# Performance work log

Measured on AMD Instinct MI355X. Metric: run time of the kernel, lower is better.

## Reference

```python
import jax, jax.numpy as jnp
import numpy as np

C = 64

def conv1x1(W, b, x):
    # W: [out, in], b: [out], x: [B, in, N, K] -> [B, out, N, K]
    return jnp.einsum('oc,bcnk->bonk', W, x) + b[None, :, None, None]

def setup_inputs() -> dict:
    key = jax.random.key(0)
    ks = jax.random.split(key, 20)
    B, N, K = 8, 4096, 16
    def w(k, o, i):
        # kaiming-uniform-ish init like torch Conv2d default
        bound = 1.0 / np.sqrt(i)
        return jax.random.uniform(k, (o, i), jnp.float32, -bound, bound)
    def bias(k, o, i):
        bound = 1.0 / np.sqrt(i)
        return jax.random.uniform(k, (o,), jnp.float32, -bound, bound)
    inp = {
        'grouped_xyz': jax.random.normal(ks[0], (B, 3, N, K), jnp.float32),
        'grouped_feature': jax.random.normal(ks[1], (B, C, N, K), jnp.float32),
        'kW': w(ks[2], C, C), 'kb': bias(ks[3], C, C),
        'vW': w(ks[4], C, C), 'vb': bias(ks[5], C, C),
        'pm1W': w(ks[6], C, 3), 'pm1b': bias(ks[7], C, 3),
        'pm2W': w(ks[8], C, C), 'pm2b': bias(ks[9], C, C),
        'pb1W': w(ks[10], C, 3), 'pb1b': bias(ks[11], C, 3),
        'pb2W': w(ks[12], C, C), 'pb2b': bias(ks[13], C, C),
        'we1W': w(ks[14], C, C), 'we1b': bias(ks[15], C, C),
        'we2W': w(ks[16], C, C), 'we2b': bias(ks[17], C, C),
        'resW': w(ks[18], C, C), 'resb': bias(ks[19], C, C),
    }
    return inp

def reference(grouped_xyz, grouped_feature, kW, kb, vW, vb,
              pm1W, pm1b, pm2W, pm2b, pb1W, pb1b, pb2W, pb2b,
              we1W, we1b, we2W, we2b, resW, resb):
    key = conv1x1(kW, kb, grouped_feature)
    value = conv1x1(vW, vb, grouped_feature)
    # positional-encoding multiplier and bias (Conv-ReLU-Conv on xyz)
    pem = conv1x1(pm2W, pm2b, jax.nn.relu(conv1x1(pm1W, pm1b, grouped_xyz)))
    peb = conv1x1(pb2W, pb2b, jax.nn.relu(conv1x1(pb1W, pb1b, grouped_xyz)))
    relation_qk = key * pem + peb
    value = value + peb
    weight = conv1x1(we2W, we2b, jax.nn.relu(conv1x1(we1W, we1b, relation_qk)))
    score = jax.nn.softmax(weight, axis=2)  # softmax over npoint dim, as in source
    feature = score * value
    # residual_emb: ReLU then 1x1 conv
    return conv1x1(resW, resb, jax.nn.relu(feature))
```

## Files before the change

### kernel.cpp

```cpp
#include <hip/hip_runtime.h>
#include <hip/hip_fp16.h>

#define NKr 65536
#define LOG2E 1.44269504f

typedef __attribute__((ext_vector_type(4))) float f32x4;
typedef __attribute__((ext_vector_type(8))) short s16x8;

__device__ __forceinline__ short bfc(float x){
    union{float f; unsigned u;} a; a.f = x;
    unsigned r = a.u + 0x7fffu + ((a.u >> 16) & 1u);
    return (short)(r >> 16);
}
__device__ __forceinline__ short hfc(float x){
    __half h = __float2half(x);
    return *(short*)&h;
}
__device__ __forceinline__ float hdec(unsigned short s){
    __half h = *(__half*)&s;
    return __half2float(h);
}

__global__ void k0_kernel(const float* __restrict__ pm1W, const float* __restrict__ pb1W,
                          const float* __restrict__ pm2W, const float* __restrict__ pb2W,
                          const float* __restrict__ kW,   const float* __restrict__ vW,
                          const float* __restrict__ we1W, const float* __restrict__ we2W,
                          const float* __restrict__ resW, short* __restrict__ wbf)
{
    const int tg = blockIdx.x * 256 + threadIdx.x;
    for (int i = tg; i < 32768; i += 16384){
        short v;
        if (i < 2048){
            const int o = i >> 5, c = i & 31;
            v = (c < 3) ? bfc(pm1W[o*3 + c]) : (short)0;
        } else if (i < 4096){
            const int ii = i - 2048, o = ii >> 5, c = ii & 31;
            v = (c < 3) ? bfc(pb1W[o*3 + c]) : (short)0;
        } else {
            const int m = (i - 4096) >> 12, j = (i - 4096) & 4095;
            const float* s = (m == 0) ? pm2W : (m == 1) ? pb2W : (m == 2) ? kW
                           : (m == 3) ? vW   : (m == 4) ? we1W : (m == 5) ? we2W : resW;
            v = bfc(s[j]);
        }
        wbf[i] = v;
    }
}

__device__ __forceinline__ void gemm64(const short* __restrict__ S,
                                       const short* __restrict__ wbf, int wo,
                                       const float* __restrict__ bias,
                                       int li, int hi, f32x4 acc[4][4])
{
#pragma unroll
    for (int mi = 0; mi < 4; ++mi){
        const float4 bv = *(const float4*)(bias + 16*mi + 4*hi);
#pragma unroll
        for (int ni = 0; ni < 4; ++ni){
            acc[mi][ni][0] = bv.x; acc[mi][ni][1] = bv.y;
            acc[mi][ni][2] = bv.z; acc[mi][ni][3] = bv.w;
        }
    }
#pragma unroll
    for (int ks = 0; ks < 2; ++ks){
        s16x8 af[4];
#pragma unroll
        for (int mi = 0; mi < 4; ++mi)
            af[mi] = *(const s16x8*)(wbf + wo + (16*mi + li)*64 + ks*32 + hi*8);
#pragma unroll
        for (int ni = 0; ni < 4; ++ni){
            const int p = 16*ni + li;
            const s16x8 bf_ = *(const s16x8*)(S + ((p*64 + ks*32 + hi*8) ^ ((li & 7) << 3)));
#pragma unroll
            for (int mi = 0; mi < 4; ++mi)
                acc[mi][ni] = __builtin_amdgcn_mfma_f32_16x16x32_bf16(af[mi], bf_, acc[mi][ni], 0, 0, 0);
        }
    }
}

__device__ __forceinline__ void gemm32x(const s16x8* __restrict__ xf,
                                        const short* __restrict__ wbf, int wo,
                                        const float* __restrict__ bias,
                                        int li, int hi, f32x4 acc[4][4])
{
#pragma unroll
    for (int mi = 0; mi < 4; ++mi){
        const float4 bv = *(const float4*)(bias + 16*mi + 4*hi);
#pragma unroll
        for (int ni = 0; ni < 4; ++ni){
            acc[mi][ni][0] = bv.x; acc[mi][ni][1] = bv.y;
            acc[mi][ni][2] = bv.z; acc[mi][ni][3] = bv.w;
        }
    }
    s16x8 af[4];
#pragma unroll
    for (int mi = 0; mi < 4; ++mi)
        af[mi] = *(const s16x8*)(wbf + wo + (16*mi + li)*32 + hi*8);
#pragma unroll
    for (int ni = 0; ni < 4; ++ni)
#pragma unroll
        for (int mi = 0; mi < 4; ++mi)
            acc[mi][ni] = __builtin_amdgcn_mfma_f32_16x16x32_bf16(af[mi], xf[ni], acc[mi][ni], 0, 0, 0);
}

__device__ __forceinline__ void dstore_bf(short* __restrict__ Tt, f32x4 acc[4][4],
                                          int li, int hi, bool relu)
{
#pragma unroll
    for (int mi = 0; mi < 4; ++mi){
        const int o0 = 16*mi + 4*hi;
#pragma unroll
        for (int ni = 0; ni < 4; ++ni){
            const int p = 16*ni + li;
            float a0 = acc[mi][ni][0], a1 = acc[mi][ni][1];
            float a2 = acc[mi][ni][2], a3 = acc[mi][ni][3];
            if (relu){ a0 = fmaxf(a0, 0.f); a1 = fmaxf(a1, 0.f);
                       a2 = fmaxf(a2, 0.f); a3 = fmaxf(a3, 0.f); }
            uint2 pk;
            pk.x = (unsigned)(unsigned short)bfc(a0) | ((unsigned)(unsigned short)bfc(a1) << 16);
            pk.y = (unsigned)(unsigned short)bfc(a2) | ((unsigned)(unsigned short)bfc(a3) << 16);
            *(uint2*)(Tt + ((p*64 + o0) ^ ((li & 7) << 3))) = pk;
        }
    }
}

__device__ __forceinline__ void dstore_h16(short* __restrict__ Tt, f32x4 acc[4][4],
                                           int li, int hi)
{
#pragma unroll
    for (int mi = 0; mi < 4; ++mi){
        const int o0 = 16*mi + 4*hi;
#pragma unroll
        for (int ni = 0; ni < 4; ++ni){
            const int p = 16*ni + li;
            uint2 pk;
            pk.x = (unsigned)(unsigned short)hfc(acc[mi][ni][0]) | ((unsigned)(unsigned short)hfc(acc[mi][ni][1]) << 16);
            pk.y = (unsigned)(unsigned short)hfc(acc[mi][ni][2]) | ((unsigned)(unsigned short)hfc(acc[mi][ni][3]) << 16);
            *(uint2*)(Tt + ((p*64 + o0) ^ ((li & 7) << 3))) = pk;
        }
    }
}

__device__ __forceinline__ void tstore(const short* __restrict__ Tt, short* __restrict__ gout, int l)
{
#pragma unroll
    for (int g = 0; g < 8; ++g){
        uint4 d = *(const uint4*)(Tt + ((l*64 + g*8) ^ ((l & 7) << 3)));
        *(uint4*)(gout + g*8) = d;
    }
}

__global__ void __launch_bounds__(64, 4) k1_kernel(
    const float* __restrict__ xyz, const float* __restrict__ feat,
    const short* __restrict__ wbf,
    const float* __restrict__ kb,  const float* __restrict__ vb,
    const float* __restrict__ pm1b, const float* __restrict__ pm2b,
    const float* __restrict__ pb1b, const float* __restrict__ pb2b,
    const float* __restrict__ we1b, const float* __restrict__ we2b,
    short* __restrict__ o_val2, short* __restrict__ o_wgt)
{
    __shared__ short Fs[4096];
    __shared__ short Ts[4096];
    const int l = threadIdx.x;
    const int li = l & 15, hi = l >> 4;
    short* F = Fs;
    short* T = Ts;
    const int b = blockIdx.x >> 10;
    const int rbase = (blockIdx.x & 1023) << 6;

    {
        const float* fb = feat + (size_t)(b * 64) * NKr + rbase + l;
#pragma unroll 4
        for (int c0 = 0; c0 < 64; c0 += 8){
            short v[8];
#pragma unroll
            for (int j = 0; j < 8; ++j) v[j] = bfc(fb[(size_t)(c0 + j) * NKr]);
            uint4 pk;
            pk.x = (unsigned)(unsigned short)v[0] | ((unsigned)(unsigned short)v[1] << 16);
            pk.y = (unsigned)(unsigned short)v[2] | ((unsigned)(unsigned short)v[3] << 16);
            pk.z = (unsigned)(unsigned short)v[4] | ((unsigned)(unsigned short)v[5] << 16);
            pk.w = (unsigned)(unsigned short)v[6] | ((unsigned)(unsigned short)v[7] << 16);
            *(uint4*)(F + ((l*64 + c0) ^ ((l & 7) << 3))) = pk;
        }
    }
    s16x8 xf[4];
#pragma unroll
    for (int ni = 0; ni < 4; ++ni)
#pragma unroll
        for (int j = 0; j < 8; ++j) xf[ni][j] = 0;
    if (hi == 0){
        const float* xb = xyz + (size_t)(b * 3) * NKr + rbase;
#pragma unroll
        for (int ni = 0; ni < 4; ++ni){
            const int p = 16*ni + li;
            xf[ni][0] = bfc(xb[p]);
            xf[ni][1] = bfc(xb[NKr + p]);
            xf[ni][2] = bfc(xb[2*NKr + p]);
        }
    }

    f32x4 A1[4][4], A2[4][4];
    gemm64(F, wbf, 12288, kb, li, hi, A1);
    gemm32x(xf, wbf, 0, pm1b, li, hi, A2);
    dstore_bf(T, A2, li, hi, true);
    gemm64(T, wbf, 4096, pm2b, li, hi, A2);
#pragma unroll
    for (int mi = 0; mi < 4; ++mi)
#pragma unroll
        for (int ni = 0; ni < 4; ++ni)
#pragma unroll
            for (int j = 0; j < 4; ++j) A1[mi][ni][j] *= A2[mi][ni][j];
    gemm32x(xf, wbf, 2048, pb1b, li, hi, A2);
    dstore_bf(T, A2, li, hi, true);
    gemm64(T, wbf, 8192, pb2b, li, hi, A2);
#pragma unroll
    for (int mi = 0; mi < 4; ++mi)
#pragma unroll
        for (int ni = 0; ni < 4; ++ni)
#pragma unroll
            for (int j = 0; j < 4; ++j) A1[mi][ni][j] += A2[mi][ni][j];
    dstore_bf(T, A1, li, hi, false);
    gemm64(F, wbf, 16384, vb, li, hi, A1);
#pragma unroll
    for (int mi = 0; mi < 4; ++mi)
#pragma unroll
        for (int ni = 0; ni < 4; ++ni)
#pragma unroll
            for (int j = 0; j < 4; ++j) A1[mi][ni][j] += A2[mi][ni][j];
    dstore_h16(F, A1, li, hi);
    const size_t rowoff = ((size_t)b * NKr + rbase + l) * 64;
    tstore(F, o_val2 + rowoff, l);
    gemm64(T, wbf, 20480, we1b, li, hi, A1);
    dstore_bf(F, A1, li, hi, true);
    gemm64(F, wbf, 24576, we2b, li, hi, A1);
    dstore_h16(T, A1, li, hi);
    tstore(T, o_wgt + rowoff, l);
}

__device__ __forceinline__ void comb(float& m, float& S, float mo, float So)
{
    float mn = fmaxf(m, mo);
    S = S * exp2f((m - mn) * LOG2E) + So * exp2f((mo - mn) * LOG2E);
    m = mn;
}

__global__ void __launch_bounds__(512) k2_kernel(const short* __restrict__ wgt,
                                                 float* __restrict__ mstat,
                                                 float* __restrict__ rstat)
{
    __shared__ float redm[8][4][8], reds[8][4][8];
    const int blk = blockIdx.x;
    const int b = blk >> 5, k = (blk >> 1) & 15, h = blk & 1;
    const int t = threadIdx.x;
    const int oct = t & 3, g = t >> 2;
    const short* wp = wgt + (size_t)b * NKr * 64 + (size_t)k * 64 + h * 32 + oct * 8;

    float m[8], S[8];
#pragma unroll
    for (int j = 0; j < 8; ++j){ m[j] = -3.0e38f; S[j] = 0.f; }
#pragma unroll 2
    for (int i = 0; i < 32; ++i){
        const int n = g + 128 * i;
        const uint4 u = *(const uint4*)(wp + (size_t)n * 1024);
        unsigned short hs[8] = {
            (unsigned short)(u.x & 0xffffu), (unsigned short)(u.x >> 16),
            (unsigned short)(u.y & 0xffffu), (unsigned short)(u.y >> 16),
            (unsigned short)(u.z & 0xffffu), (unsigned short)(u.z >> 16),
            (unsigned short)(u.w & 0xffffu), (unsigned short)(u.w >> 16)};
#pragma unroll
        for (int j = 0; j < 8; ++j){
            const float x = hdec(hs[j]);
            const float mn = fmaxf(m[j], x);
            S[j] = S[j] * exp2f((m[j] - mn) * LOG2E) + exp2f((x - mn) * LOG2E);
            m[j] = mn;
        }
    }
#pragma unroll
    for (int d = 4; d <= 32; d <<= 1){
#pragma unroll
        for (int j = 0; j < 8; ++j){
            float mo = __shfl_xor(m[j], d, 64);
            float So = __shfl_xor(S[j], d, 64);
            comb(m[j], S[j], mo, So);
        }
    }
    const int wv = t >> 6, ln = t & 63;
    if (ln < 4){
#pragma unroll
        for (int j = 0; j < 8; ++j){ redm[wv][ln][j] = m[j]; reds[wv][ln][j] = S[j]; }
    }
    __syncthreads();
    if (t < 32){
        const int oc = t >> 3, j = t & 7;
        float M = redm[0][oc][j], Sm = reds[0][oc][j];
#pragma unroll
        for (int wv2 = 1; wv2 < 8; ++wv2) comb(M, Sm, redm[wv2][oc][j], reds[wv2][oc][j]);
        const int idx = (b * 16 + k) * 64 + h * 32 + oc * 8 + j;
        mstat[idx] = M;
        rstat[idx] = 1.0f / Sm;
    }
}

__global__ void __launch_bounds__(64, 4) k3_kernel(
    const short* __restrict__ wgt, const short* __restrict__ val2,
    const float* __restrict__ mstat, const float* __restrict__ rstat,
    const short* __restrict__ wbf, const float* __restrict__ resb,
    float* __restrict__ out)
{
    __shared__ short ftile[4096];
    __shared__ float mls[1024], rls[1024];
    const int l = threadIdx.x;
    const int li = l & 15, hi = l >> 4;
    const int b = blockIdx.x >> 10;
    const int rbase = (blockIdx.x & 1023) << 6;

    {
        const float* mp = mstat + b * 1024;
        const float* rp = rstat + b * 1024;
#pragma unroll
        for (int i = 0; i < 16; ++i){
            const int f = l + 64 * i;
            const int kk = f >> 6;
            const int fs = f ^ ((kk & 7) << 2);
            mls[fs] = mp[f];
            rls[fs] = rp[f];
        }
    }
    __syncthreads();

    short* Ft = ftile;
    const int k = l & 15;
    const size_t rowoff = ((size_t)b * NKr + rbase + l) * 64;
    const short* wp = wgt + rowoff;
    const short* vp = val2 + rowoff;
#pragma unroll 2
    for (int g = 0; g < 8; ++g){
        const uint4 uw = *(const uint4*)(wp + g * 8);
        const uint4 uv = *(const uint4*)(vp + g * 8);
        const int f0 = (k * 64 + g * 8) ^ ((k & 7) << 2);
        const int f1 = (k * 64 + g * 8 + 4) ^ ((k & 7) << 2);
        const float4 m0 = *(const float4*)(mls + f0);
        const float4 m1 = *(const float4*)(mls + f1);
        const float4 r0 = *(const float4*)(rls + f0);
        const float4 r1 = *(const float4*)(rls + f1);
        const unsigned short ws8[8] = {
            (unsigned short)(uw.x & 0xffffu), (unsigned short)(uw.x >> 16),
            (unsigned short)(uw.y & 0xffffu), (unsigned short)(uw.y >> 16),
            (unsigned short)(uw.z & 0xffffu), (unsigned short)(uw.z >> 16),
            (unsigned short)(uw.w & 0xffffu), (unsigned short)(uw.w >> 16)};
        const unsigned short vs8[8] = {
            (unsigned short)(uv.x & 0xffffu), (unsigned short)(uv.x >> 16),
            (unsigned short)(uv.y & 0xffffu), (unsigned short)(uv.y >> 16),
            (unsigned short)(uv.z & 0xffffu), (unsigned short)(uv.z >> 16),
            (unsigned short)(uv.w & 0xffffu), (unsigned short)(uv.w >> 16)};
        const float mv[8] = {m0.x, m0.y, m0.z, m0.w, m1.x, m1.y, m1.z, m1.w};
        const float rv[8] = {r0.x, r0.y, r0.z, r0.w, r1.x, r1.y, r1.z, r1.w};
        short fo[8];
#pragma unroll
        for (int j = 0; j < 8; ++j){
            const float sc = exp2f((hdec(ws8[j]) - mv[j]) * LOG2E) * rv[j];
            fo[j] = bfc(fmaxf(sc * hdec(vs8[j]), 0.f));
        }
        uint4 pk;
        pk.x = (unsigned)(unsigned short)fo[0] | ((unsigned)(unsigned short)fo[1] << 16);
        pk.y = (unsigned)(unsigned short)fo[2] | ((unsigned)(unsigned short)fo[3] << 16);
        pk.z = (unsigned)(unsigned short)fo[4] | ((unsigned)(unsigned short)fo[5] << 16);
        pk.w = (unsigned)(unsigned short)fo[6] | ((unsigned)(unsigned short)fo[7] << 16);
        *(uint4*)(Ft + ((l * 64 + g * 8) ^ ((l & 7) << 3))) = pk;
    }
    f32x4 acc[4][4];
    gemm64(Ft, wbf, 28672, resb, li, hi, acc);
    float* op = out + (size_t)b * 64 * NKr;
#pragma unroll
    for (int mi = 0; mi < 4; ++mi){
        const int o0 = 16 * mi + 4 * hi;
#pragma unroll
        for (int ni = 0; ni < 4; ++ni){
            const int r = rbase + 16 * ni + li;
#pragma unroll
            for (int j = 0; j < 4; ++j)
                op[(size_t)(o0 + j) * NKr + r] = acc[mi][ni][j];
        }
    }
}

extern "C" void kernel_launch(void* const* d_in, const int* in_sizes, int n_in,
                              void* d_out, int out_size, void* d_ws, size_t ws_size,
                              hipStream_t stream)
{
    const float* xyz  = (const float*)d_in[0];
    const float* feat = (const float*)d_in[1];
    const float* kW   = (const float*)d_in[2];  const float* kb   = (const float*)d_in[3];
    const float* vW   = (const float*)d_in[4];  const float* vb   = (const float*)d_in[5];
    const float* pm1W = (const float*)d_in[6];  const float* pm1b = (const float*)d_in[7];
    const float* pm2W = (const float*)d_in[8];  const float* pm2b = (const float*)d_in[9];
    const float* pb1W = (const float*)d_in[10]; const float* pb1b = (const float*)d_in[11];
    const float* pb2W = (const float*)d_in[12]; const float* pb2b = (const float*)d_in[13];
    const float* we1W = (const float*)d_in[14]; const float* we1b = (const float*)d_in[15];
    const float* we2W = (const float*)d_in[16]; const float* we2b = (const float*)d_in[17];
    const float* resW = (const float*)d_in[18]; const float* resb = (const float*)d_in[19];

    short* wbf   = (short*)d_ws;
    float* mstat = (float*)((char*)d_ws + 65536);
    float* rstat = (float*)((char*)d_ws + 98304);
    short* val2  = (short*)((char*)d_ws + 131072);
    short* wgt   = (short*)((char*)d_ws + 131072 + 67108864);

    k0_kernel<<<64, 256, 0, stream>>>(pm1W, pb1W, pm2W, pb2W, kW, vW, we1W, we2W, resW, wbf);
    k1_kernel<<<8192, 64, 0, stream>>>(xyz, feat, wbf, kb, vb, pm1b, pm2b,
                                       pb1b, pb2b, we1b, we2b, val2, wgt);
    k2_kernel<<<256, 512, 0, stream>>>(wgt, mstat, rstat);
    k3_kernel<<<8192, 64, 0, stream>>>(wgt, val2, mstat, rstat, wbf, resb, (float*)d_out);
}
```

Measured before the change: 437.9 us.

## Split 64-row tiles across four waves per block in k1 and k3

The k1 and k3 kernels change from one 64-thread wave per 64-point tile to 256-thread blocks. Each of the four waves computes 16 of the 64 output channels through new per-wave GEMM and store helpers, with __syncthreads between the chained GEMM stages. k3 drops its shared-memory staging of the softmax statistics and reads them directly as float4 per thread, and k1 keeps value results in a third shared buffer. The intent is to cut per-thread accumulator register pressure and get more parallel waves per tile, at the cost of extra barriers and smaller MFMA work per wave.

After: 380.6 us. 1.15x faster.

```diff
diff --git a/kernel.cpp b/kernel.cpp
--- a/kernel.cpp
+++ b/kernel.cpp
@@ -46,110 +46,72 @@
     }
 }
 
-__device__ __forceinline__ void gemm64(const short* __restrict__ S,
-                                       const short* __restrict__ wbf, int wo,
-                                       const float* __restrict__ bias,
-                                       int li, int hi, f32x4 acc[4][4])
-{
-#pragma unroll
-    for (int mi = 0; mi < 4; ++mi){
-        const float4 bv = *(const float4*)(bias + 16*mi + 4*hi);
-#pragma unroll
-        for (int ni = 0; ni < 4; ++ni){
-            acc[mi][ni][0] = bv.x; acc[mi][ni][1] = bv.y;
-            acc[mi][ni][2] = bv.z; acc[mi][ni][3] = bv.w;
-        }
-    }
-#pragma unroll
-    for (int ks = 0; ks < 2; ++ks){
-        s16x8 af[4];
-#pragma unroll
-        for (int mi = 0; mi < 4; ++mi)
-            af[mi] = *(const s16x8*)(wbf + wo + (16*mi + li)*64 + ks*32 + hi*8);
-#pragma unroll
-        for (int ni = 0; ni < 4; ++ni){
-            const int p = 16*ni + li;
-            const s16x8 bf_ = *(const s16x8*)(S + ((p*64 + ks*32 + hi*8) ^ ((li & 7) << 3)));
-#pragma unroll
-            for (int mi = 0; mi < 4; ++mi)
-                acc[mi][ni] = __builtin_amdgcn_mfma_f32_16x16x32_bf16(af[mi], bf_, acc[mi][ni], 0, 0, 0);
-        }
-    }
-}
-
-__device__ __forceinline__ void gemm32x(const s16x8* __restrict__ xf,
+__device__ __forceinline__ void sgemm64(const short* __restrict__ S,
                                         const short* __restrict__ wbf, int wo,
                                         const float* __restrict__ bias,
-                                        int li, int hi, f32x4 acc[4][4])
-{
-#pragma unroll
-    for (int mi = 0; mi < 4; ++mi){
-        const float4 bv = *(const float4*)(bias + 16*mi + 4*hi);
+                                        int w, int li, int hi, f32x4 acc[4])
+{
+    const float4 bv = *(const float4*)(bias + 16*w + 4*hi);
+#pragma unroll
+    for (int ni = 0; ni < 4; ++ni){
+        acc[ni][0] = bv.x; acc[ni][1] = bv.y; acc[ni][2] = bv.z; acc[ni][3] = bv.w;
+    }
+#pragma unroll
+    for (int ks = 0; ks < 2; ++ks){
+        const s16x8 af = *(const s16x8*)(wbf + wo + (16*w + li)*64 + ks*32 + hi*8);
 #pragma unroll
         for (int ni = 0; ni < 4; ++ni){
-            acc[mi][ni][0] = bv.x; acc[mi][ni][1] = bv.y;
-            acc[mi][ni][2] = bv.z; acc[mi][ni][3] = bv.w;
-        }
-    }
-    s16x8 af[4];
-#pragma unroll
-    for (int mi = 0; mi < 4; ++mi)
-        af[mi] = *(const s16x8*)(wbf + wo + (16*mi + li)*32 + hi*8);
+            const s16x8 bf_ = *(const s16x8*)(S + (((16*ni + li)*64 + ks*32 + hi*8) ^ ((li & 7) << 3)));
+            acc[ni] = __builtin_amdgcn_mfma_f32_16x16x32_bf16(af, bf_, acc[ni], 0, 0, 0);
+        }
+    }
+}
+
+__device__ __forceinline__ void sgemm32x(const s16x8* __restrict__ xf,
+                                         const short* __restrict__ wbf, int wo,
+                                         const float* __restrict__ bias,
+                                         int w, int li, int hi, f32x4 acc[4])
+{
+    const float4 bv = *(const float4*)(bias + 16*w + 4*hi);
+#pragma unroll
+    for (int ni = 0; ni < 4; ++ni){
+        acc[ni][0] = bv.x; acc[ni][1] = bv.y; acc[ni][2] = bv.z; acc[ni][3] = bv.w;
+    }
+    const s16x8 af = *(const s16x8*)(wbf + wo + (16*w + li)*32 + hi*8);
 #pragma unroll
     for (int ni = 0; ni < 4; ++ni)
-#pragma unroll
-        for (int mi = 0; mi < 4; ++mi)
-            acc[mi][ni] = __builtin_amdgcn_mfma_f32_16x16x32_bf16(af[mi], xf[ni], acc[mi][ni], 0, 0, 0);
-}
-
-__device__ __forceinline__ void dstore_bf(short* __restrict__ Tt, f32x4 acc[4][4],
-                                          int li, int hi, bool relu)
-{
-#pragma unroll
-    for (int mi = 0; mi < 4; ++mi){
-        const int o0 = 16*mi + 4*hi;
-#pragma unroll
-        for (int ni = 0; ni < 4; ++ni){
-            const int p = 16*ni + li;
-            float a0 = acc[mi][ni][0], a1 = acc[mi][ni][1];
-            float a2 = acc[mi][ni][2], a3 = acc[mi][ni][3];
-            if (relu){ a0 = fmaxf(a0, 0.f); a1 = fmaxf(a1, 0.f);
-                       a2 = fmaxf(a2, 0.f); a3 = fmaxf(a3, 0.f); }
-            uint2 pk;
-            pk.x = (unsigned)(unsigned short)bfc(a0) | ((unsigned)(unsigned short)bfc(a1) << 16);
-            pk.y = (unsigned)(unsigned short)bfc(a2) | ((unsigned)(unsigned short)bfc(a3) << 16);
-            *(uint2*)(Tt + ((p*64 + o0) ^ ((li & 7) << 3))) = pk;
-        }
-    }
-}
-
-__device__ __forceinline__ void dstore_h16(short* __restrict__ Tt, f32x4 acc[4][4],
-                                           int li, int hi)
-{
-#pragma unroll
-    for (int mi = 0; mi < 4; ++mi){
-        const int o0 = 16*mi + 4*hi;
-#pragma unroll
-        for (int ni = 0; ni < 4; ++ni){
-            const int p = 16*ni + li;
-            uint2 pk;
-            pk.x = (unsigned)(unsigned short)hfc(acc[mi][ni][0]) | ((unsigned)(unsigned short)hfc(acc[mi][ni][1]) << 16);
-            pk.y = (unsigned)(unsigned short)hfc(acc[mi][ni][2]) | ((unsigned)(unsigned short)hfc(acc[mi][ni][3]) << 16);
-            *(uint2*)(Tt + ((p*64 + o0) ^ ((li & 7) << 3))) = pk;
-        }
-    }
-}
-
-__device__ __forceinline__ void tstore(const short* __restrict__ Tt, short* __restrict__ gout, int l)
-{
-#pragma unroll
-    for (int g = 0; g < 8; ++g){
-        uint4 d = *(const uint4*)(Tt + ((l*64 + g*8) ^ ((l & 7) << 3)));
-        *(uint4*)(gout + g*8) = d;
-    }
-}
-
-__global__ void __launch_bounds__(64, 4) k1_kernel(
+        acc[ni] = __builtin_amdgcn_mfma_f32_16x16x32_bf16(af, xf[ni], acc[ni], 0, 0, 0);
+}
+
+__device__ __forceinline__ void sdstore_bf(short* __restrict__ T, const f32x4 acc[4],
+                                           int w, int li, int hi, bool relu)
+{
+    const int o0 = 16*w + 4*hi;
+#pragma unroll
+    for (int ni = 0; ni < 4; ++ni){
+        float a0 = acc[ni][0], a1 = acc[ni][1], a2 = acc[ni][2], a3 = acc[ni][3];
+        if (relu){ a0 = fmaxf(a0,0.f); a1 = fmaxf(a1,0.f); a2 = fmaxf(a2,0.f); a3 = fmaxf(a3,0.f); }
+        uint2 pk;
+        pk.x = (unsigned)(unsigned short)bfc(a0) | ((unsigned)(unsigned short)bfc(a1) << 16);
+        pk.y = (unsigned)(unsigned short)bfc(a2) | ((unsigned)(unsigned short)bfc(a3) << 16);
+        *(uint2*)(T + (((16*ni + li)*64 + o0) ^ ((li & 7) << 3))) = pk;
+    }
+}
+
+__device__ __forceinline__ void sdstore_h16(short* __restrict__ T, const f32x4 acc[4],
+                                            int w, int li, int hi)
+{
+    const int o0 = 16*w + 4*hi;
+#pragma unroll
+    for (int ni = 0; ni < 4; ++ni){
+        uint2 pk;
+        pk.x = (unsigned)(unsigned short)hfc(acc[ni][0]) | ((unsigned)(unsigned short)hfc(acc[ni][1]) << 16);
+        pk.y = (unsigned)(unsigned short)hfc(acc[ni][2]) | ((unsigned)(unsigned short)hfc(acc[ni][3]) << 16);
+        *(uint2*)(T + (((16*ni + li)*64 + o0) ^ ((li & 7) << 3))) = pk;
+    }
+}
+
+__global__ void __launch_bounds__(256, 4) k1_kernel(
     const float* __restrict__ xyz, const float* __restrict__ feat,
     const short* __restrict__ wbf,
     const float* __restrict__ kb,  const float* __restrict__ vb,
@@ -158,29 +120,32 @@
     const float* __restrict__ we1b, const float* __restrict__ we2b,
     short* __restrict__ o_val2, short* __restrict__ o_wgt)
 {
-    __shared__ short Fs[4096];
-    __shared__ short Ts[4096];
-    const int l = threadIdx.x;
+    __shared__ short F[4096];
+    __shared__ short T[4096];
+    __shared__ short Vt[4096];
+    const int tid = threadIdx.x;
+    const int w = tid >> 6, l = tid & 63;
     const int li = l & 15, hi = l >> 4;
-    short* F = Fs;
-    short* T = Ts;
     const int b = blockIdx.x >> 10;
     const int rbase = (blockIdx.x & 1023) << 6;
 
     {
-        const float* fb = feat + (size_t)(b * 64) * NKr + rbase + l;
-#pragma unroll 4
-        for (int c0 = 0; c0 < 64; c0 += 8){
-            short v[8];
-#pragma unroll
-            for (int j = 0; j < 8; ++j) v[j] = bfc(fb[(size_t)(c0 + j) * NKr]);
-            uint4 pk;
-            pk.x = (unsigned)(unsigned short)v[0] | ((unsigned)(unsigned short)v[1] << 16);
-            pk.y = (unsigned)(unsigned short)v[2] | ((unsigned)(unsigned short)v[3] << 16);
-            pk.z = (unsigned)(unsigned short)v[4] | ((unsigned)(unsigned short)v[5] << 16);
-            pk.w = (unsigned)(unsigned short)v[6] | ((unsigned)(unsigned short)v[7] << 16);
-            *(uint4*)(F + ((l*64 + c0) ^ ((l & 7) << 3))) = pk;
-        }
+        const float* fb = feat + ((size_t)(b*64 + 16*w)) * NKr + rbase + l;
+        short v[16];
+#pragma unroll
+        for (int j = 0; j < 16; ++j) v[j] = bfc(fb[(size_t)j * NKr]);
+        uint4 p0, p1;
+        p0.x = (unsigned)(unsigned short)v[0] | ((unsigned)(unsigned short)v[1] << 16);
+        p0.y = (unsigned)(unsigned short)v[2] | ((unsigned)(unsigned short)v[3] << 16);
+        p0.z = (unsigned)(unsigned short)v[4] | ((unsigned)(unsigned short)v[5] << 16);
+        p0.w = (unsigned)(unsigned short)v[6] | ((unsigned)(unsigned short)v[7] << 16);
+        p1.x = (unsigned)(unsigned short)v[8] | ((unsigned)(unsigned short)v[9] << 16);
+        p1.y = (unsigned)(unsigned short)v[10] | ((unsigned)(unsigned short)v[11] << 16);
+        p1.z = (unsigned)(unsigned short)v[12] | ((unsigned)(unsigned short)v[13] << 16);
+        p1.w = (unsigned)(unsigned short)v[14] | ((unsigned)(unsigned short)v[15] << 16);
+        const int s0 = l*64 + 16*w;
+        *(uint4*)(F + (s0 ^ ((l & 7) << 3))) = p0;
+        *(uint4*)(F + ((s0 + 8) ^ ((l & 7) << 3))) = p1;
     }
     s16x8 xf[4];
 #pragma unroll
@@ -188,52 +153,71 @@
 #pragma unroll
         for (int j = 0; j < 8; ++j) xf[ni][j] = 0;
     if (hi == 0){
-        const float* xb = xyz + (size_t)(b * 3) * NKr + rbase;
+        const float* xb = xyz + (size_t)(b*3) * NKr + rbase;
 #pragma unroll
         for (int ni = 0; ni < 4; ++ni){
-            const int p = 16*ni + li;
-            xf[ni][0] = bfc(xb[p]);
-            xf[ni][1] = bfc(xb[NKr + p]);
-            xf[ni][2] = bfc(xb[2*NKr + p]);
-        }
-    }
-
-    f32x4 A1[4][4], A2[4][4];
-    gemm64(F, wbf, 12288, kb, li, hi, A1);
-    gemm32x(xf, wbf, 0, pm1b, li, hi, A2);
-    dstore_bf(T, A2, li, hi, true);
-    gemm64(T, wbf, 4096, pm2b, li, hi, A2);
-#pragma unroll
-    for (int mi = 0; mi < 4; ++mi)
+            xf[ni][0] = bfc(xb[16*ni + li]);
+            xf[ni][1] = bfc(xb[NKr + 16*ni + li]);
+            xf[ni][2] = bfc(xb[2*NKr + 16*ni + li]);
+        }
+    }
+    __syncthreads();
+
+    f32x4 V[4], K[4], P[4];
+    sgemm64(F, wbf, 16384, vb, w, li, hi, V);
+    sgemm64(F, wbf, 12288, kb, w, li, hi, K);
+    sgemm32x(xf, wbf, 0, pm1b, w, li, hi, P);
+    sdstore_bf(T, P, w, li, hi, true);
+    __syncthreads();
+    sgemm64(T, wbf, 4096, pm2b, w, li, hi, P);
+#pragma unroll
+    for (int ni = 0; ni < 4; ++ni)
+#pragma unroll
+        for (int j = 0; j < 4; ++j) K[ni][j] *= P[ni][j];
+    __syncthreads();
+    sgemm32x(xf, wbf, 2048, pb1b, w, li, hi, P);
+    sdstore_bf(T, P, w, li, hi, true);
+    __syncthreads();
+    sgemm64(T, wbf, 8192, pb2b, w, li, hi, P);
+    __syncthreads();
+    {
+        f32x4 R[4];
 #pragma unroll
         for (int ni = 0; ni < 4; ++ni)
 #pragma unroll
-            for (int j = 0; j < 4; ++j) A1[mi][ni][j] *= A2[mi][ni][j];
-    gemm32x(xf, wbf, 2048, pb1b, li, hi, A2);
-    dstore_bf(T, A2, li, hi, true);
-    gemm64(T, wbf, 8192, pb2b, li, hi, A2);
-#pragma unroll
-    for (int mi = 0; mi < 4; ++mi)
+            for (int j = 0; j < 4; ++j) R[ni][j] = K[ni][j] + P[ni][j];
+        sdstore_bf(T, R, w, li, hi, false);
 #pragma unroll
         for (int ni = 0; ni < 4; ++ni)
 #pragma unroll
-            for (int j = 0; j < 4; ++j) A1[mi][ni][j] += A2[mi][ni][j];
-    dstore_bf(T, A1, li, hi, false);
-    gemm64(F, wbf, 16384, vb, li, hi, A1);
-#pragma unroll
-    for (int mi = 0; mi < 4; ++mi)
-#pragma unroll
-        for (int ni = 0; ni < 4; ++ni)
-#pragma unroll
-            for (int j = 0; j < 4; ++j) A1[mi][ni][j] += A2[mi][ni][j];
-    dstore_h16(F, A1, li, hi);
-    const size_t rowoff = ((size_t)b * NKr + rbase + l) * 64;
-    tstore(F, o_val2 + rowoff, l);
-    gemm64(T, wbf, 20480, we1b, li, hi, A1);
-    dstore_bf(F, A1, li, hi, true);
-    gemm64(F, wbf, 24576, we2b, li, hi, A1);
-    dstore_h16(T, A1, li, hi);
-    tstore(T, o_wgt + rowoff, l);
+            for (int j = 0; j < 4; ++j) R[ni][j] = V[ni][j] + P[ni][j];
+        sdstore_h16(Vt, R, w, li, hi);
+    }
+    __syncthreads();
+    {
+        const int p = tid >> 2, sub = tid & 3;
+        const int s0 = p*64 + sub*16;
+        const uint4 d0 = *(const uint4*)(Vt + (s0 ^ ((p & 7) << 3)));
+        const uint4 d1 = *(const uint4*)(Vt + ((s0 + 8) ^ ((p & 7) << 3)));
+        short* gp = o_val2 + ((size_t)b * NKr + rbase + p) * 64 + sub*16;
+        *(uint4*)gp = d0;
+        *(uint4*)(gp + 8) = d1;
+    }
+    sgemm64(T, wbf, 20480, we1b, w, li, hi, P);
+    sdstore_bf(F, P, w, li, hi, true);
+    __syncthreads();
+    sgemm64(F, wbf, 24576, we2b, w, li, hi, P);
+    sdstore_h16(Vt, P, w, li, hi);
+    __syncthreads();
+    {
+        const int p = tid >> 2, sub = tid & 3;
+        const int s0 = p*64 + sub*16;
+        const uint4 d0 = *(const uint4*)(Vt + (s0 ^ ((p & 7) << 3)));
+        const uint4 d1 = *(const uint4*)(Vt + ((s0 + 8) ^ ((p & 7) << 3)));
+        short* gp = o_wgt + ((size_t)b * NKr + rbase + p) * 64 + sub*16;
+        *(uint4*)gp = d0;
+        *(uint4*)(gp + 8) = d1;
+    }
 }
 
 __device__ __forceinline__ void comb(float& m, float& S, float mo, float So)
@@ -300,86 +284,75 @@
     }
 }
 
-__global__ void __launch_bounds__(64, 4) k3_kernel(
+__global__ void __launch_bounds__(256, 4) k3_kernel(
     const short* __restrict__ wgt, const short* __restrict__ val2,
     const float* __restrict__ mstat, const float* __restrict__ rstat,
     const short* __restrict__ wbf, const float* __restrict__ resb,
     float* __restrict__ out)
 {
-    __shared__ short ftile[4096];
-    __shared__ float mls[1024], rls[1024];
-    const int l = threadIdx.x;
-    const int li = l & 15, hi = l >> 4;
+    __shared__ short F[4096];
+    const int tid = threadIdx.x;
     const int b = blockIdx.x >> 10;
     const int rbase = (blockIdx.x & 1023) << 6;
 
     {
-        const float* mp = mstat + b * 1024;
-        const float* rp = rstat + b * 1024;
-#pragma unroll
-        for (int i = 0; i < 16; ++i){
-            const int f = l + 64 * i;
-            const int kk = f >> 6;
-            const int fs = f ^ ((kk & 7) << 2);
-            mls[fs] = mp[f];
-            rls[fs] = rp[f];
-        }
-    }
-    __syncthreads();
-
-    short* Ft = ftile;
-    const int k = l & 15;
-    const size_t rowoff = ((size_t)b * NKr + rbase + l) * 64;
-    const short* wp = wgt + rowoff;
-    const short* vp = val2 + rowoff;
-#pragma unroll 2
-    for (int g = 0; g < 8; ++g){
-        const uint4 uw = *(const uint4*)(wp + g * 8);
-        const uint4 uv = *(const uint4*)(vp + g * 8);
-        const int f0 = (k * 64 + g * 8) ^ ((k & 7) << 2);
-        const int f1 = (k * 64 + g * 8 + 4) ^ ((k & 7) << 2);
-        const float4 m0 = *(const float4*)(mls + f0);
-        const float4 m1 = *(const float4*)(mls + f1);
-        const float4 r0 = *(const float4*)(rls + f0);
-        const float4 r1 = *(const float4*)(rls + f1);
-        const unsigned short ws8[8] = {
-            (unsigned short)(uw.x & 0xffffu), (unsigned short)(uw.x >> 16),
-            (unsigned short)(uw.y & 0xffffu), (unsigned short)(uw.y >> 16),
-            (unsigned short)(uw.z & 0xffffu), (unsigned short)(uw.z >> 16),
-            (unsigned short)(uw.w & 0xffffu), (unsigned short)(uw.w >> 16)};
-        const unsigned short vs8[8] = {
-            (unsigned short)(uv.x & 0xffffu), (unsigned short)(uv.x >> 16),
-            (unsigned short)(uv.y & 0xffffu), (unsigned short)(uv.y >> 16),
-            (unsigned short)(uv.z & 0xffffu), (unsigned short)(uv.z >> 16),
-            (unsigned short)(uv.w & 0xffffu), (unsigned short)(uv.w >> 16)};
-        const float mv[8] = {m0.x, m0.y, m0.z, m0.w, m1.x, m1.y, m1.z, m1.w};
-        const float rv[8] = {r0.x, r0.y, r0.z, r0.w, r1.x, r1.y, r1.z, r1.w};
-        short fo[8];
-#pragma unroll
-        for (int j = 0; j < 8; ++j){
-            const float sc = exp2f((hdec(ws8[j]) - mv[j]) * LOG2E) * rv[j];
-            fo[j] = bfc(fmaxf(sc * hdec(vs8[j]), 0.f));
-        }
-        uint4 pk;
-        pk.x = (unsigned)(unsigned short)fo[0] | ((unsigned)(unsigned short)fo[1] << 16);
-        pk.y = (unsigned)(unsigned short)fo[2] | ((unsigned)(unsigned short)fo[3] << 16);
-        pk.z = (unsigned)(unsigned short)fo[4] | ((unsigned)(unsigned short)fo[5] << 16);
-        pk.w = (unsigned)(unsigned short)fo[6] | ((unsigned)(unsigned short)fo[7] << 16);
-        *(uint4*)(Ft + ((l * 64 + g * 8) ^ ((l & 7) << 3))) = pk;
-    }
-    f32x4 acc[4][4];
-    gemm64(Ft, wbf, 28672, resb, li, hi, acc);
+        const int p = tid >> 2, sub = tid & 3;
+        const int k = p & 15;
+        const size_t ro = ((size_t)b * NKr + rbase + p) * 64 + sub*16;
+        const uint4 uw0 = *(const uint4*)(wgt + ro);
+        const uint4 uw1 = *(const uint4*)(wgt + ro + 8);
+        const uint4 uv0 = *(const uint4*)(val2 + ro);
+        const uint4 uv1 = *(const uint4*)(val2 + ro + 8);
+        const float* mp = mstat + (b*16 + k)*64 + sub*16;
+        const float* rp = rstat + (b*16 + k)*64 + sub*16;
+        float mv[16], rv[16];
+#pragma unroll
+        for (int q = 0; q < 4; ++q){
+            const float4 mq = *(const float4*)(mp + 4*q);
+            const float4 rq = *(const float4*)(rp + 4*q);
+            mv[4*q] = mq.x; mv[4*q+1] = mq.y; mv[4*q+2] = mq.z; mv[4*q+3] = mq.w;
+            rv[4*q] = rq.x; rv[4*q+1] = rq.y; rv[4*q+2] = rq.z; rv[4*q+3] = rq.w;
+        }
+        const unsigned uu[8] = {uw0.x, uw0.y, uw0.z, uw0.w, uw1.x, uw1.y, uw1.z, uw1.w};
+        const unsigned vv[8] = {uv0.x, uv0.y, uv0.z, uv0.w, uv1.x, uv1.y, uv1.z, uv1.w};
+        short fo[16];
+#pragma unroll
+        for (int e = 0; e < 8; ++e){
+            const float w0 = hdec((unsigned short)(uu[e] & 0xffffu));
+            const float w1 = hdec((unsigned short)(uu[e] >> 16));
+            const float v0 = hdec((unsigned short)(vv[e] & 0xffffu));
+            const float v1 = hdec((unsigned short)(vv[e] >> 16));
+            const float s0 = exp2f((w0 - mv[2*e]) * LOG2E) * rv[2*e];
+            const float s1 = exp2f((w1 - mv[2*e+1]) * LOG2E) * rv[2*e+1];
+            fo[2*e]   = bfc(fmaxf(s0 * v0, 0.f));
+            fo[2*e+1] = bfc(fmaxf(s1 * v1, 0.f));
+        }
+        uint4 p0, p1;
+        p0.x = (unsigned)(unsigned short)fo[0] | ((unsigned)(unsigned short)fo[1] << 16);
+        p0.y = (unsigned)(unsigned short)fo[2] | ((unsigned)(unsigned short)fo[3] << 16);
+        p0.z = (unsigned)(unsigned short)fo[4] | ((unsigned)(unsigned short)fo[5] << 16);
+        p0.w = (unsigned)(unsigned short)fo[6] | ((unsigned)(unsigned short)fo[7] << 16);
+        p1.x = (unsigned)(unsigned short)fo[8] | ((unsigned)(unsigned short)fo[9] << 16);
+        p1.y = (unsigned)(unsigned short)fo[10] | ((unsigned)(unsigned short)fo[11] << 16);
+        p1.z = (unsigned)(unsigned short)fo[12] | ((unsigned)(unsigned short)fo[13] << 16);
+        p1.w = (unsigned)(unsigned short)fo[14] | ((unsigned)(unsigned short)fo[15] << 16);
+        const int s0i = p*64 + sub*16;
+        *(uint4*)(F + (s0i ^ ((p & 7) << 3))) = p0;
+        *(uint4*)(F + ((s0i + 8) ^ ((p & 7) << 3))) = p1;
+    }
+    __syncthreads();
+
+    const int w = tid >> 6, l = tid & 63;
+    const int li = l & 15, hi = l >> 4;
+    f32x4 acc[4];
+    sgemm64(F, wbf, 28672, resb, w, li, hi, acc);
     float* op = out + (size_t)b * 64 * NKr;
 #pragma unroll
-    for (int mi = 0; mi < 4; ++mi){
-        const int o0 = 16 * mi + 4 * hi;
-#pragma unroll
-        for (int ni = 0; ni < 4; ++ni){
-            const int r = rbase + 16 * ni + li;
-#pragma unroll
-            for (int j = 0; j < 4; ++j)
-                op[(size_t)(o0 + j) * NKr + r] = acc[mi][ni][j];
-        }
+    for (int ni = 0; ni < 4; ++ni){
+        const int r = rbase + 16*ni + li;
+#pragma unroll
+        for (int j = 0; j < 4; ++j)
+            op[(size_t)(16*w + 4*hi + j) * NKr + r] = acc[ni][j];
     }
 }
 
@@ -406,8 +379,8 @@
     short* wgt   = (short*)((char*)d_ws + 131072 + 67108864);
 
     k0_kernel<<<64, 256, 0, stream>>>(pm1W, pb1W, pm2W, pb2W, kW, vW, we1W, we2W, resW, wbf);
-    k1_kernel<<<8192, 64, 0, stream>>>(xyz, feat, wbf, kb, vb, pm1b, pm2b,
-                                       pb1b, pb2b, we1b, we2b, val2, wgt);
+    k1_kernel<<<8192, 256, 0, stream>>>(xyz, feat, wbf, kb, vb, pm1b, pm2b,
+                                        pb1b, pb2b, we1b, we2b, val2, wgt);
     k2_kernel<<<256, 512, 0, stream>>>(wgt, mstat, rstat);
-    k3_kernel<<<8192, 64, 0, stream>>>(wgt, val2, mstat, rstat, wbf, resb, (float*)d_out);
-}
+    k3_kernel<<<8192, 256, 0, stream>>>(wgt, val2, mstat, rstat, wbf, resb, (float*)d_out);
+}
```
